# Kernel optimization log

Hardware: AMD Instinct MI355X
Metric: run time of the kernel (lower is better)

The kernel has to match this reference:

```python
import jax, jax.numpy as jnp
import numpy as np

B, C, H, W = 8, 128, 64, 64


def setup_inputs() -> dict:
    key = jax.random.key(0)
    ks = jax.random.split(key, 7)
    query_img = jax.random.normal(ks[0], (B, C, H, W), dtype=jnp.float32)
    key_img = jax.random.normal(ks[1], (B, C, H, W), dtype=jnp.float32)
    value_img = jax.random.normal(ks[2], (B, C, H, W), dtype=jnp.float32)
    # 1x1 conv weights == dense [out, in] matrices (kaiming-ish scale)
    scale = 1.0 / np.sqrt(C)
    Wq = jax.random.normal(ks[3], (C, C), dtype=jnp.float32) * scale
    bq = jax.random.normal(ks[4], (C,), dtype=jnp.float32) * scale
    Wk = jax.random.normal(ks[5], (C, C), dtype=jnp.float32) * scale
    bk = jax.random.normal(ks[6], (C,), dtype=jnp.float32) * scale
    return {"query_img": query_img, "key_img": key_img, "value_img": value_img,
            "Wq": Wq, "bq": bq, "Wk": Wk, "bk": bk}


def reference(query_img, key_img, value_img, Wq, bq, Wk, bk):
    b, c, h, w = query_img.shape
    hw = h * w
    # 1x1 convs as GEMMs -> token-major layout (b, hw, c_out)
    q = jnp.einsum('bchw,oc->bhwo', query_img, Wq).reshape(b, hw, -1) + bq
    k = jnp.einsum('bchw,oc->bohw', key_img, Wk).reshape(b, -1, hw) + bk[None, :, None]
    # scores scaled by sqrt(HW) (faithful: key.size(-1) == h*w in source)
    scores = jnp.einsum('bqc,bck->bqk', q, k) / jnp.sqrt(jnp.float32(hw))
    attn = jax.nn.softmax(scores, axis=-1)  # (b, hw, hw)
    v = value_img.reshape(b, c, hw).transpose(0, 2, 1)  # (b, hw, c)
    out = jnp.einsum('bqk,bkc->bqc', attn, v)  # (b, hw, c)
    out = out.transpose(0, 2, 1).reshape(b, -1, h, w)
    out = out + q.transpose(0, 2, 1).reshape(b, -1, h, w)  # residual from query proj
    return out
```

## Files before the change

### kernel.cpp

```cpp
#include <hip/hip_runtime.h>

#define BB 8
#define CC 128
#define SS 4096
#define KT 64
#define SCALE 0.015625f

typedef __attribute__((ext_vector_type(8))) short sh8;
typedef __attribute__((ext_vector_type(4))) float f32x4;

__device__ __forceinline__ float b2f(unsigned short u) {
    union { unsigned int i; float f; } x; x.i = ((unsigned int)u) << 16; return x.f;
}
__device__ __forceinline__ unsigned short f2b(float f) {
    union { float f; unsigned int i; } x; x.f = f;
    unsigned int r = x.i + 0x7fff + ((x.i >> 16) & 1);
    return (unsigned short)(r >> 16);
}
__device__ __forceinline__ unsigned short rhu(float f) {
    union { float f; unsigned int i; } x; x.f = f;
    return (unsigned short)((x.i + 0x8000) >> 16);
}

__device__ __forceinline__ void dma16(const void* g, void* l) {
    __builtin_amdgcn_global_load_lds((const __attribute__((address_space(1))) void*)g,
                                     (__attribute__((address_space(3))) void*)l,
                                     16, 0, 0);
}

__global__ __launch_bounds__(256) void aux_kernel(
    const float* __restrict__ qimg, const float* __restrict__ kimg,
    const float* __restrict__ vimg,
    const float* __restrict__ Wq, const float* __restrict__ bq,
    const float* __restrict__ Wk, const float* __restrict__ bk,
    unsigned short* __restrict__ Qbuf, unsigned short* __restrict__ Kbuf,
    unsigned short* __restrict__ Vbuf)
{
    const int tid = threadIdx.x;
    const int z   = blockIdx.z;

    if (z == 2) {
        const size_t base = ((size_t)blockIdx.y * 64 + blockIdx.x) * 8192 + tid * 4;
        #pragma unroll
        for (int it = 0; it < 8; ++it) {
            const size_t i = base + (size_t)it * 1024;
            float4 v = *(const float4*)(vimg + i);
            ushort4 o;
            o.x = f2b(v.x); o.y = f2b(v.y); o.z = f2b(v.z); o.w = f2b(v.w);
            *(ushort4*)(Vbuf + i) = o;
        }
        return;
    }

    __shared__ float ilds[128 * 69];

    const float* img  = (z == 0) ? qimg : kimg;
    const float* Wf   = (z == 0) ? Wq : Wk;
    const float* bias = (z == 0) ? bq : bk;
    unsigned short* outTok = (z == 0) ? Qbuf : Kbuf;

    const int wave = tid >> 6;
    const int lane = tid & 63;
    const int l15  = lane & 15;
    const int quad = lane >> 4;
    const int b     = blockIdx.y;
    const int stile = blockIdx.x;

    const float* gbase = img + (size_t)b * CC * SS + stile * 64;
    #pragma unroll
    for (int i = 0; i < 8; ++i) {
        const int l = tid + 256 * i;
        const int row = l >> 4, col = (l & 15) * 4;
        float4 v = *(const float4*)(gbase + (size_t)row * SS + col);
        float* d = ilds + row * 69 + col;
        d[0] = v.x; d[1] = v.y; d[2] = v.z; d[3] = v.w;
    }
    __syncthreads();

    const int tcol = wave * 16 + l15;
    sh8 a[4];
    #pragma unroll
    for (int kk = 0; kk < 4; ++kk)
        #pragma unroll
        for (int j = 0; j < 8; ++j)
            a[kk][j] = (short)rhu(ilds[(32 * kk + quad * 8 + j) * 69 + tcol]);

    f32x4 acc[8];
    #pragma unroll
    for (int nt = 0; nt < 8; ++nt) acc[nt] = (f32x4){0.f, 0.f, 0.f, 0.f};

    #pragma unroll
    for (int nt = 0; nt < 8; ++nt) {
        const float* wp = Wf + (size_t)(16 * nt + l15) * CC + quad * 8;
        #pragma unroll
        for (int kk = 0; kk < 4; ++kk) {
            float4 w0 = *(const float4*)(wp + 32 * kk);
            float4 w1 = *(const float4*)(wp + 32 * kk + 4);
            sh8 bfr;
            bfr[0] = (short)rhu(w0.x); bfr[1] = (short)rhu(w0.y);
            bfr[2] = (short)rhu(w0.z); bfr[3] = (short)rhu(w0.w);
            bfr[4] = (short)rhu(w1.x); bfr[5] = (short)rhu(w1.y);
            bfr[6] = (short)rhu(w1.z); bfr[7] = (short)rhu(w1.w);
            acc[nt] = __builtin_amdgcn_mfma_f32_16x16x32_bf16(a[kk], bfr, acc[nt], 0, 0, 0);
        }
    }

    #pragma unroll
    for (int nt = 0; nt < 8; ++nt) {
        const int o = 16 * nt + l15;
        const float bv = bias[o];
        #pragma unroll
        for (int r = 0; r < 4; ++r) {
            const int s = stile * 64 + wave * 16 + quad * 4 + r;
            outTok[((size_t)b * SS + s) * CC + o] = f2b(acc[nt][r] + bv);
        }
    }
}

__global__ __launch_bounds__(256, 2) void attn_kernel(
    const unsigned short* __restrict__ Qbuf,
    const unsigned short* __restrict__ Kbuf,
    const unsigned short* __restrict__ Vbuf,
    float* __restrict__ out)
{
    __shared__ __align__(16) unsigned char smem[73728];

    const int tid  = threadIdx.x;
    const int wave = tid >> 6;
    const int lane = tid & 63;
    const int l15  = lane & 15;
    const int quad = lane >> 4;
    const int b     = blockIdx.y;
    const int qtile = blockIdx.x;
    const int qbase = qtile * 64 + wave * 16;

    unsigned char* pw = smem + 65536 + wave * 2048;

    const unsigned short* kbp = Kbuf + (size_t)b * SS * CC;
    const unsigned short* vbp = Vbuf + (size_t)b * CC * SS;

    sh8 aq[4];
    {
        const unsigned short* qp = Qbuf + ((size_t)b * SS + qbase + l15) * CC + quad * 8;
        #pragma unroll
        for (int kk = 0; kk < 4; ++kk) aq[kk] = *(const sh8*)(qp + 32 * kk);
    }

    int kGO[4], vGO[4];
    #pragma unroll
    for (int j = 0; j < 4; ++j) {
        const int krow = wave * 16 + j * 4 + (lane >> 4);
        kGO[j] = krow * 256 + (((lane & 15) ^ (krow & 7)) << 4);
        const int vrow = (wave * 4 + j) * 8 + (lane >> 3);
        vGO[j] = vrow * 8192 + (((lane & 7) ^ ((lane >> 3) & 7)) << 4);
    }

    f32x4 oacc[8];
    #pragma unroll
    for (int ct = 0; ct < 8; ++ct) oacc[ct] = (f32x4){0.f, 0.f, 0.f, 0.f};
    float lsum[4] = {0.f, 0.f, 0.f, 0.f};

    #pragma unroll
    for (int j = 0; j < 4; ++j) {
        dma16((const char*)kbp + kGO[j], smem + (wave * 4 + j) * 1024);
        dma16((const char*)vbp + vGO[j], smem + 32768 + (wave * 4 + j) * 1024);
    }

    for (int it = 0; it < SS / KT; ++it) {
        const int cur = (it & 1) * 16384;
        unsigned char* kb = smem + cur;
        unsigned char* vb = smem + 32768 + cur;

        __syncthreads();

        if (it + 1 < SS / KT) {
            const int nxt = 16384 - cur;
            const char* gk = (const char*)kbp + (size_t)(it + 1) * KT * 256;
            const char* gv = (const char*)vbp + (size_t)(it + 1) * KT * 2;
            #pragma unroll
            for (int j = 0; j < 4; ++j) {
                dma16(gk + kGO[j], smem + nxt + (wave * 4 + j) * 1024);
                dma16(gv + vGO[j], smem + 32768 + nxt + (wave * 4 + j) * 1024);
            }
        }

        f32x4 sacc[4];
        #pragma unroll
        for (int n = 0; n < 4; ++n) {
            sacc[n] = (f32x4){0.f, 0.f, 0.f, 0.f};
            #pragma unroll
            for (int kk = 0; kk < 4; ++kk) {
                sh8 kf = *(const sh8*)(kb + (16 * n + l15) * 256
                                          + (((4 * kk + quad) ^ (l15 & 7)) << 4));
                sacc[n] = __builtin_amdgcn_mfma_f32_16x16x32_bf16(aq[kk], kf, sacc[n], 0, 0, 0);
            }
        }

        #pragma unroll
        for (int n = 0; n < 4; ++n)
            #pragma unroll
            for (int r = 0; r < 4; ++r) {
                float p = __expf(sacc[n][r] * SCALE);
                lsum[r] += p;
                const int row = quad * 4 + r, col = 16 * n + l15;
                *(unsigned short*)(pw + row * 128
                                   + (((col >> 3) ^ (row & 7)) << 4)
                                   + (col & 7) * 2) = rhu(p);
            }

        #pragma unroll
        for (int ks = 0; ks < 2; ++ks) {
            sh8 ap = *(const sh8*)(pw + l15 * 128
                                   + (((4 * ks + quad) ^ (l15 & 7)) << 4));
            #pragma unroll
            for (int ct = 0; ct < 8; ++ct) {
                sh8 bv = *(const sh8*)(vb + (16 * ct + l15) * 128
                                          + (((4 * ks + quad) ^ (l15 & 7)) << 4));
                oacc[ct] = __builtin_amdgcn_mfma_f32_16x16x32_bf16(ap, bv, oacc[ct], 0, 0, 0);
            }
        }
    }

    #pragma unroll
    for (int r = 0; r < 4; ++r) {
        float v = lsum[r];
        #pragma unroll
        for (int m = 8; m >= 1; m >>= 1) v += __shfl_xor(v, m, 64);
        lsum[r] = v;
    }

    __syncthreads();

    float (*oLds)[129] = (float(*)[129])smem;
    #pragma unroll
    for (int ct = 0; ct < 8; ++ct) {
        const int c = 16 * ct + l15;
        #pragma unroll
        for (int r = 0; r < 4; ++r) {
            const int qloc  = wave * 16 + quad * 4 + r;
            const int qglob = qtile * 64 + qloc;
            const float resid = b2f(Qbuf[((size_t)b * SS + qglob) * CC + c]);
            oLds[qloc][c] = oacc[ct][r] / lsum[r] + resid;
        }
    }
    __syncthreads();
    for (int idx = tid; idx < 64 * 128; idx += 256) {
        const int c = idx >> 6, q = idx & 63;
        out[((size_t)b * CC + c) * SS + qtile * 64 + q] = oLds[q][c];
    }
}

extern "C" void kernel_launch(void* const* d_in, const int* in_sizes, int n_in,
                              void* d_out, int out_size, void* d_ws, size_t ws_size,
                              hipStream_t stream) {
    const float* qimg = (const float*)d_in[0];
    const float* kimg = (const float*)d_in[1];
    const float* vimg = (const float*)d_in[2];
    const float* Wq   = (const float*)d_in[3];
    const float* bq   = (const float*)d_in[4];
    const float* Wk   = (const float*)d_in[5];
    const float* bk   = (const float*)d_in[6];
    float* out = (float*)d_out;

    unsigned short* Qbuf = (unsigned short*)d_ws;
    unsigned short* Kbuf = Qbuf + (size_t)BB * SS * CC;
    unsigned short* Vbuf = Kbuf + (size_t)BB * SS * CC;

    aux_kernel<<<dim3(SS / 64, BB, 3), 256, 0, stream>>>(
        qimg, kimg, vimg, Wq, bq, Wk, bk, Qbuf, Kbuf, Vbuf);
    attn_kernel<<<dim3(SS / 64, BB), 256, 0, stream>>>(Qbuf, Kbuf, Vbuf, out);
}
```

Baseline: 228.0 us.

## Switch attention kernel to 32x32x16 MFMA with cross-wave shared P tile

Restructures the attention inner loop to use 32x32x16 bf16 MFMAs. Each pair of waves now splits a 32-query half of the tile, one wave per 32-key half for QK^T and one per 64-channel half for PV. The softmax probabilities go into a block-shared LDS tile with a new XOR layout, so an extra __syncthreads per iteration is needed. Partial row sums are combined across waves through LDS at the end, and exp uses exp2f with a log2e-folded scale. The aim is fewer LDS fragment reads per MFMA, but the added barrier and changed K/V layout assumptions (no swizzle on K/V loads) may cause bank conflicts.

```diff
diff --git a/kernel.cpp b/kernel.cpp
--- a/kernel.cpp
+++ b/kernel.cpp
@@ -4,10 +4,11 @@
 #define CC 128
 #define SS 4096
 #define KT 64
-#define SCALE 0.015625f
-
-typedef __attribute__((ext_vector_type(8))) short sh8;
-typedef __attribute__((ext_vector_type(4))) float f32x4;
+#define SCL2 0.022542120f
+
+typedef __attribute__((ext_vector_type(8)))  short sh8;
+typedef __attribute__((ext_vector_type(4)))  float f32x4;
+typedef __attribute__((ext_vector_type(16))) float f32x16;
 
 __device__ __forceinline__ float b2f(unsigned short u) {
     union { unsigned int i; float f; } x; x.i = ((unsigned int)u) << 16; return x.f;
@@ -123,47 +124,51 @@
     const unsigned short* __restrict__ Vbuf,
     float* __restrict__ out)
 {
-    __shared__ __align__(16) unsigned char smem[73728];
+    __shared__ __align__(16) unsigned char smem[74240];
+    unsigned char* pLds  = smem + 65536;
+    float* lsumsLds      = (float*)(smem + 73728);
 
     const int tid  = threadIdx.x;
     const int wave = tid >> 6;
     const int lane = tid & 63;
-    const int l15  = lane & 15;
-    const int quad = lane >> 4;
+    const int l31  = lane & 31;
+    const int h    = lane >> 5;
+    const int qh    = wave >> 1;
+    const int kth   = wave & 1;
+    const int chalf = wave & 1;
     const int b     = blockIdx.y;
     const int qtile = blockIdx.x;
-    const int qbase = qtile * 64 + wave * 16;
-
-    unsigned char* pw = smem + 65536 + wave * 2048;
-
-    const unsigned short* kbp = Kbuf + (size_t)b * SS * CC;
-    const unsigned short* vbp = Vbuf + (size_t)b * CC * SS;
-
-    sh8 aq[4];
+
+    const char* kbp = (const char*)(Kbuf + (size_t)b * SS * CC);
+    const char* vbp = (const char*)(Vbuf + (size_t)b * CC * SS);
+
+    sh8 aq[8];
     {
-        const unsigned short* qp = Qbuf + ((size_t)b * SS + qbase + l15) * CC + quad * 8;
-        #pragma unroll
-        for (int kk = 0; kk < 4; ++kk) aq[kk] = *(const sh8*)(qp + 32 * kk);
+        const unsigned short* qp = Qbuf + ((size_t)b * SS + qtile * 64 + 32 * qh + l31) * CC + 8 * h;
+        #pragma unroll
+        for (int ks = 0; ks < 8; ++ks) aq[ks] = *(const sh8*)(qp + 16 * ks);
     }
 
     int kGO[4], vGO[4];
     #pragma unroll
     for (int j = 0; j < 4; ++j) {
-        const int krow = wave * 16 + j * 4 + (lane >> 4);
-        kGO[j] = krow * 256 + (((lane & 15) ^ (krow & 7)) << 4);
-        const int vrow = (wave * 4 + j) * 8 + (lane >> 3);
-        vGO[j] = vrow * 8192 + (((lane & 7) ^ ((lane >> 3) & 7)) << 4);
-    }
-
-    f32x4 oacc[8];
-    #pragma unroll
-    for (int ct = 0; ct < 8; ++ct) oacc[ct] = (f32x4){0.f, 0.f, 0.f, 0.f};
-    float lsum[4] = {0.f, 0.f, 0.f, 0.f};
+        kGO[j] = lane * 256 + (wave * 4 + j) * 16;
+        vGO[j] = (64 * (j & 1) + lane) * 8192 + (2 * wave + (j >> 1)) * 16;
+    }
+
+    f32x16 oacc[2];
+    #pragma unroll
+    for (int ct = 0; ct < 2; ++ct)
+        #pragma unroll
+        for (int r = 0; r < 16; ++r) oacc[ct][r] = 0.f;
+    float lsum[16];
+    #pragma unroll
+    for (int r = 0; r < 16; ++r) lsum[r] = 0.f;
 
     #pragma unroll
     for (int j = 0; j < 4; ++j) {
-        dma16((const char*)kbp + kGO[j], smem + (wave * 4 + j) * 1024);
-        dma16((const char*)vbp + vGO[j], smem + 32768 + (wave * 4 + j) * 1024);
+        dma16(kbp + kGO[j], smem + (wave * 4 + j) * 1024);
+        dma16(vbp + vGO[j], smem + 32768 + (wave * 4 + j) * 1024);
     }
 
     for (int it = 0; it < SS / KT; ++it) {
@@ -175,8 +180,8 @@
 
         if (it + 1 < SS / KT) {
             const int nxt = 16384 - cur;
-            const char* gk = (const char*)kbp + (size_t)(it + 1) * KT * 256;
-            const char* gv = (const char*)vbp + (size_t)(it + 1) * KT * 2;
+            const char* gk = kbp + (size_t)(it + 1) * 16384;
+            const char* gv = vbp + (size_t)(it + 1) * 128;
             #pragma unroll
             for (int j = 0; j < 4; ++j) {
                 dma16(gk + kGO[j], smem + nxt + (wave * 4 + j) * 1024);
@@ -184,63 +189,70 @@
             }
         }
 
-        f32x4 sacc[4];
-        #pragma unroll
-        for (int n = 0; n < 4; ++n) {
-            sacc[n] = (f32x4){0.f, 0.f, 0.f, 0.f};
+        f32x16 sacc;
+        #pragma unroll
+        for (int r = 0; r < 16; ++r) sacc[r] = 0.f;
+        #pragma unroll
+        for (int ks = 0; ks < 8; ++ks) {
+            sh8 kf = *(const sh8*)(kb + (2 * ks + h) * 1024 + (32 * kth + l31) * 16);
+            sacc = __builtin_amdgcn_mfma_f32_32x32x16_bf16(aq[ks], kf, sacc, 0, 0, 0);
+        }
+
+        {
+            const int ktcw = 4 * kth + (l31 >> 3);
+            const int k7o  = (l31 & 7) * 2;
+            unsigned char* pb = pLds + ktcw * 1024 + qh * 512 + k7o;
             #pragma unroll
-            for (int kk = 0; kk < 4; ++kk) {
-                sh8 kf = *(const sh8*)(kb + (16 * n + l15) * 256
-                                          + (((4 * kk + quad) ^ (l15 & 7)) << 4));
-                sacc[n] = __builtin_amdgcn_mfma_f32_16x16x32_bf16(aq[kk], kf, sacc[n], 0, 0, 0);
+            for (int reg = 0; reg < 16; ++reg) {
+                float p = exp2f(sacc[reg] * SCL2);
+                lsum[reg] += p;
+                const int q31 = (reg & 3) + 8 * (reg >> 2) + 4 * h;
+                *(unsigned short*)(pb + ((q31 ^ ktcw) << 4)) = rhu(p);
             }
         }
 
-        #pragma unroll
-        for (int n = 0; n < 4; ++n)
+        __syncthreads();
+
+        #pragma unroll
+        for (int ks = 0; ks < 4; ++ks) {
+            const int ktc = 2 * ks + h;
+            sh8 ap = *(const sh8*)(pLds + ktc * 1024 + qh * 512 + ((l31 ^ ktc) << 4));
             #pragma unroll
-            for (int r = 0; r < 4; ++r) {
-                float p = __expf(sacc[n][r] * SCALE);
-                lsum[r] += p;
-                const int row = quad * 4 + r, col = 16 * n + l15;
-                *(unsigned short*)(pw + row * 128
-                                   + (((col >> 3) ^ (row & 7)) << 4)
-                                   + (col & 7) * 2) = rhu(p);
+            for (int ct = 0; ct < 2; ++ct) {
+                sh8 bv = *(const sh8*)(vb + ktc * 2048 + (64 * chalf + 32 * ct + l31) * 16);
+                oacc[ct] = __builtin_amdgcn_mfma_f32_32x32x16_bf16(ap, bv, oacc[ct], 0, 0, 0);
             }
-
-        #pragma unroll
-        for (int ks = 0; ks < 2; ++ks) {
-            sh8 ap = *(const sh8*)(pw + l15 * 128
-                                   + (((4 * ks + quad) ^ (l15 & 7)) << 4));
-            #pragma unroll
-            for (int ct = 0; ct < 8; ++ct) {
-                sh8 bv = *(const sh8*)(vb + (16 * ct + l15) * 128
-                                          + (((4 * ks + quad) ^ (l15 & 7)) << 4));
-                oacc[ct] = __builtin_amdgcn_mfma_f32_16x16x32_bf16(ap, bv, oacc[ct], 0, 0, 0);
-            }
-        }
-    }
-
-    #pragma unroll
-    for (int r = 0; r < 4; ++r) {
-        float v = lsum[r];
-        #pragma unroll
-        for (int m = 8; m >= 1; m >>= 1) v += __shfl_xor(v, m, 64);
-        lsum[r] = v;
-    }
-
+        }
+    }
+
+    #pragma unroll
+    for (int reg = 0; reg < 16; ++reg) {
+        float v = lsum[reg];
+        #pragma unroll
+        for (int m = 16; m >= 1; m >>= 1) v += __shfl_xor(v, m, 64);
+        lsum[reg] = v;
+    }
+    if (l31 == 0) {
+        #pragma unroll
+        for (int reg = 0; reg < 16; ++reg) {
+            const int r31 = (reg & 3) + 8 * (reg >> 2) + 4 * h;
+            lsumsLds[(qh * 2 + kth) * 32 + r31] = lsum[reg];
+        }
+    }
     __syncthreads();
 
-    float (*oLds)[129] = (float(*)[129])smem;
-    #pragma unroll
-    for (int ct = 0; ct < 8; ++ct) {
-        const int c = 16 * ct + l15;
-        #pragma unroll
-        for (int r = 0; r < 4; ++r) {
-            const int qloc  = wave * 16 + quad * 4 + r;
-            const int qglob = qtile * 64 + qloc;
-            const float resid = b2f(Qbuf[((size_t)b * SS + qglob) * CC + c]);
-            oLds[qloc][c] = oacc[ct][r] / lsum[r] + resid;
+    float (*oLds)[132] = (float(*)[132])smem;
+    #pragma unroll
+    for (int ct = 0; ct < 2; ++ct) {
+        const int ch = 64 * chalf + 32 * ct + l31;
+        #pragma unroll
+        for (int reg = 0; reg < 16; ++reg) {
+            const int r31  = (reg & 3) + 8 * (reg >> 2) + 4 * h;
+            const int qloc = 32 * qh + r31;
+            const float lt = lsumsLds[(qh * 2 + 0) * 32 + r31]
+                           + lsumsLds[(qh * 2 + 1) * 32 + r31];
+            const float resid = b2f(Qbuf[((size_t)b * SS + qtile * 64 + qloc) * CC + ch]);
+            oLds[qloc][ch] = oacc[ct][reg] / lt + resid;
         }
     }
     __syncthreads();
```

Result: slower. 285.7 us (+25.3%).
